# Kernel optimization log

Hardware: AMD Instinct MI355X
Metric: run time of the kernel (lower is better)

## Reference

```python
import jax, jax.numpy as jnp
import numpy as np

D_MODEL = 1024
D_KEY = 64
BATCH = 4
SEQ = 4096


def setup_inputs() -> dict:
    key = jax.random.key(0)
    kq, kk, kv, kwq, kwk, kwv = jax.random.split(key, 6)
    queries = jax.random.normal(kq, (BATCH, SEQ, D_MODEL), dtype=jnp.float32)
    keys = jax.random.normal(kk, (BATCH, SEQ, D_MODEL), dtype=jnp.float32)
    values = jax.random.normal(kv, (BATCH, SEQ, D_MODEL), dtype=jnp.float32)
    # causal mask: 1 = keep, 0 = masked out (torch masked_fill where mask==0)
    mask = jnp.tril(jnp.ones((SEQ, SEQ), dtype=jnp.int32))
    s = 1.0 / np.sqrt(D_MODEL)
    Wq = jax.random.normal(kwq, (D_MODEL, D_KEY), dtype=jnp.float32) * s
    Wk = jax.random.normal(kwk, (D_MODEL, D_KEY), dtype=jnp.float32) * s
    Wv = jax.random.normal(kwv, (D_MODEL, D_KEY), dtype=jnp.float32) * s
    return {"queries": queries, "keys": keys, "values": values,
            "mask": mask, "Wq": Wq, "Wk": Wk, "Wv": Wv}


def reference(queries, keys, values, mask, Wq, Wk, Wv):
    q = jnp.einsum('bsd,dk->bsk', queries, Wq)   # [B,S,dk]
    k = jnp.einsum('bsd,dk->bsk', keys, Wk)
    v = jnp.einsum('bsd,dk->bsk', values, Wv)
    scale = 1.0 / np.sqrt(D_KEY).astype(np.float32)
    attn = jnp.einsum('bqk,bsk->bqs', q, k) * scale  # [B,Sq,Sk]
    attn = jnp.where(mask == 0, -jnp.inf, attn)
    attn = jax.nn.softmax(attn, axis=-1)
    return jnp.einsum('bqs,bsk->bqk', attn, v)      # [B,S,dk]
```

## Files before the change

### kernel.cpp

```cpp
#include <hip/hip_runtime.h>
#include <hip/hip_bf16.h>

#define B      4
#define SEQ    4096
#define DM     1024
#define DK     64
#define NSPLIT 8

typedef __bf16 bf16x8 __attribute__((ext_vector_type(8)));
typedef __bf16 bf16x4 __attribute__((ext_vector_type(4)));
typedef float  f32x4  __attribute__((ext_vector_type(4)));

#define KSTR 72

#define QSCALE 0.1803368801111204f
#define M2BIAS 12.0f

__device__ __forceinline__ void gl_lds16(const void* g, void* l)
{
    __builtin_amdgcn_global_load_lds(
        (const __attribute__((address_space(1))) void*)g,
        (__attribute__((address_space(3))) void*)l, 16, 0, 0);
}

__global__ __launch_bounds__(256) void wt_kernel(
    const float* __restrict__ Wq, const float* __restrict__ Wk,
    const float* __restrict__ Wv, __bf16* __restrict__ Wt)
{
    const int mat = blockIdx.y;
    const float* W = (mat == 0) ? Wq : (mat == 1) ? Wk : Wv;
    const float scale = (mat == 0) ? QSCALE : 1.0f;
    const int k0 = blockIdx.x * 64;
    const int tid = threadIdx.x;

    __shared__ float t[64][65];

    const int r = tid >> 2;
    const int c = (tid & 3) * 16;
    {
        const float* src = W + (size_t)(k0 + r) * DK + c;
        #pragma unroll
        for (int j = 0; j < 4; ++j) {
            float4 a = *(const float4*)(src + j * 4);
            t[r][c + j * 4 + 0] = a.x; t[r][c + j * 4 + 1] = a.y;
            t[r][c + j * 4 + 2] = a.z; t[r][c + j * 4 + 3] = a.w;
        }
    }
    __syncthreads();
    const int n  = tid >> 2;
    const int kk = (tid & 3) * 16;
    bf16x8 b0, b1;
    #pragma unroll
    for (int j = 0; j < 8; ++j) b0[j] = (__bf16)(t[kk + j][n] * scale);
    #pragma unroll
    for (int j = 0; j < 8; ++j) b1[j] = (__bf16)(t[kk + 8 + j][n] * scale);
    __bf16* dst = Wt + (size_t)(mat * DK + n) * DM + k0 + kk;
    *(bf16x8*)(dst)     = b0;
    *(bf16x8*)(dst + 8) = b1;
}

__global__ __launch_bounds__(256) void proj_lds_kernel(
    const float* __restrict__ q_in, const float* __restrict__ k_in,
    const float* __restrict__ v_in, const __bf16* __restrict__ Wt,
    __bf16* __restrict__ qb, __bf16* __restrict__ kb,
    __bf16* __restrict__ vtb)
{
    const int m = blockIdx.y;
    const float* in = (m == 0) ? q_in : (m == 1) ? k_in : v_in;
    const __bf16* wt = Wt + (size_t)m * DK * DM;

    const int rowbase = blockIdx.x * 64;
    const int tid  = threadIdx.x;
    const int w    = tid >> 6;
    const int lane = tid & 63;
    const int quad = lane >> 4;
    const int l15  = lane & 15;

    __shared__ float  As[2][64 * 64];
    __shared__ __bf16 Ws[2][64 * 64];

    const float* asrc[4];
    #pragma unroll
    for (int i = 0; i < 4; ++i) {
        const int j = w * 4 + i;
        const int row_local = j * 4 + quad;
        asrc[i] = in + (size_t)(rowbase + row_local) * DM
                     + ((l15 ^ (row_local & 7)) << 2);
    }
    const __bf16* wsrc[2];
    const int l8 = lane >> 3, u7 = lane & 7;
    #pragma unroll
    for (int i = 0; i < 2; ++i) {
        const int j2 = w * 2 + i;
        const int n_local = j2 * 8 + l8;
        wsrc[i] = wt + (size_t)n_local * DM + ((u7 ^ (n_local & 7)) << 3);
    }

    auto stage = [&](int b, int c) {
        #pragma unroll
        for (int i = 0; i < 4; ++i)
            gl_lds16(asrc[i] + c * 64, &As[b][(w * 4 + i) * 256]);
        #pragma unroll
        for (int i = 0; i < 2; ++i)
            gl_lds16(wsrc[i] + c * 64, &Ws[b][(w * 2 + i) * 512]);
    };

    f32x4 acc[4];
    #pragma unroll
    for (int nf = 0; nf < 4; ++nf) acc[nf] = (f32x4){0.f, 0.f, 0.f, 0.f};

    stage(0, 0);

    const int row = w * 16 + l15;
    const int sw7 = l15 & 7;

    for (int c = 0; c < 16; ++c) {
        __syncthreads();
        if (c + 1 < 16) stage((c + 1) & 1, c + 1);
        const int b = c & 1;

        #pragma unroll
        for (int s = 0; s < 2; ++s) {
            const int q0 = s * 8 + quad * 2;
            float4 a0 = *(const float4*)&As[b][row * 64 + (( q0      ^ sw7) << 2)];
            float4 a1 = *(const float4*)&As[b][row * 64 + (((q0 + 1) ^ sw7) << 2)];
            bf16x8 af;
            af[0] = (__bf16)a0.x; af[1] = (__bf16)a0.y;
            af[2] = (__bf16)a0.z; af[3] = (__bf16)a0.w;
            af[4] = (__bf16)a1.x; af[5] = (__bf16)a1.y;
            af[6] = (__bf16)a1.z; af[7] = (__bf16)a1.w;
            #pragma unroll
            for (int nf = 0; nf < 4; ++nf) {
                const int n = nf * 16 + l15;
                bf16x8 wf = *(const bf16x8*)
                    &Ws[b][n * 64 + (((s * 4 + quad) ^ sw7) << 3)];
                acc[nf] = __builtin_amdgcn_mfma_f32_16x16x32_bf16(af, wf, acc[nf], 0, 0, 0);
            }
        }
    }

    if (m < 2) {
        __bf16* outb = (m == 0) ? qb : kb;
        #pragma unroll
        for (int nf = 0; nf < 4; ++nf)
            #pragma unroll
            for (int r = 0; r < 4; ++r)
                outb[(size_t)(rowbase + w * 16 + quad * 4 + r) * DK + nf * 16 + l15] =
                    (__bf16)acc[nf][r];
    } else {
        const int bb = rowbase >> 12;
        const int s0 = (rowbase & (SEQ - 1)) + w * 16 + quad * 4;
        #pragma unroll
        for (int nf = 0; nf < 4; ++nf) {
            bf16x4 v4;
            #pragma unroll
            for (int r = 0; r < 4; ++r) v4[r] = (__bf16)acc[nf][r];
            *(bf16x4*)&vtb[(size_t)(bb * DK + nf * 16 + l15) * SEQ + s0] = v4;
        }
    }
}

__global__ __launch_bounds__(256) void flash_kernel(
    const __bf16* __restrict__ qb, const __bf16* __restrict__ kb,
    const __bf16* __restrict__ vtb, __bf16* __restrict__ Opart,
    float* __restrict__ lpart)
{
    const int qt  = blockIdx.x;
    const int bb  = blockIdx.y;
    const int z   = blockIdx.z;
    const int tid = threadIdx.x;
    const int w    = tid >> 6;
    const int lane = tid & 63;
    const int quad = lane >> 4;
    const int l15  = lane & 15;

    __shared__ __bf16 Ks[64 * KSTR];
    __shared__ __bf16 Vs[64 * KSTR];
    __shared__ __bf16 Ps[4][2][16 * KSTR];

    const int qrow_base = qt * 128 + w * 32;
    const int niters = 2 * qt + 2;
    const int kt0 = (niters * z) / NSPLIT;
    const int kt1 = (niters * (z + 1)) / NSPLIT;

    bf16x8 qf[2][2];
    #pragma unroll
    for (int g = 0; g < 2; ++g) {
        const __bf16* qp = qb + ((size_t)(bb * SEQ + qrow_base + g * 16 + l15)) * DK + quad * 8;
        qf[g][0] = *(const bf16x8*)(qp);
        qf[g][1] = *(const bf16x8*)(qp + 32);
    }

    bf16x8 ones;
    #pragma unroll
    for (int j = 0; j < 8; ++j) ones[j] = (__bf16)1.0f;

    f32x4 of[2][4], lacc[2];
    #pragma unroll
    for (int g = 0; g < 2; ++g) {
        #pragma unroll
        for (int nf = 0; nf < 4; ++nf) of[g][nf] = (f32x4){0.f, 0.f, 0.f, 0.f};
        lacc[g] = (f32x4){0.f, 0.f, 0.f, 0.f};
    }

    const int sr = tid >> 2;
    const int sc = (tid & 3) * 16;
    bf16x8 kr0, kr1, vr0, vr1;
    const __bf16* kbase = kb  + ((size_t)(bb * SEQ + sr)) * DK + sc;
    const __bf16* vbase = vtb + ((size_t)(bb * DK  + sr)) * SEQ + sc;

    if (kt1 > kt0) {
        const __bf16* kg = kbase + (size_t)kt0 * 64 * DK;
        kr0 = *(const bf16x8*)(kg); kr1 = *(const bf16x8*)(kg + 8);
        const __bf16* vg = vbase + kt0 * 64;
        vr0 = *(const bf16x8*)(vg); vr1 = *(const bf16x8*)(vg + 8);
    }

    for (int kt = kt0; kt < kt1; ++kt) {
        __syncthreads();
        *(bf16x8*)&Ks[sr * KSTR + sc]     = kr0;
        *(bf16x8*)&Ks[sr * KSTR + sc + 8] = kr1;
        *(bf16x8*)&Vs[sr * KSTR + sc]     = vr0;
        *(bf16x8*)&Vs[sr * KSTR + sc + 8] = vr1;
        __syncthreads();
        if (kt + 1 < kt1) {
            const __bf16* kg = kbase + (size_t)(kt + 1) * 64 * DK;
            kr0 = *(const bf16x8*)(kg); kr1 = *(const bf16x8*)(kg + 8);
            const __bf16* vg = vbase + (kt + 1) * 64;
            vr0 = *(const bf16x8*)(vg); vr1 = *(const bf16x8*)(vg + 8);
        }

        f32x4 sf[2][4];
        #pragma unroll
        for (int g = 0; g < 2; ++g)
            #pragma unroll
            for (int nf = 0; nf < 4; ++nf)
                sf[g][nf] = (f32x4){-M2BIAS, -M2BIAS, -M2BIAS, -M2BIAS};
        #pragma unroll
        for (int nf = 0; nf < 4; ++nf) {
            #pragma unroll
            for (int ch = 0; ch < 2; ++ch) {
                bf16x8 kf = *(const bf16x8*)(&Ks[(nf * 16 + l15) * KSTR + ch * 32 + quad * 8]);
                sf[0][nf] = __builtin_amdgcn_mfma_f32_16x16x32_bf16(qf[0][ch], kf, sf[0][nf], 0, 0, 0);
                sf[1][nf] = __builtin_amdgcn_mfma_f32_16x16x32_bf16(qf[1][ch], kf, sf[1][nf], 0, 0, 0);
            }
        }

        const int kc0 = kt * 64;
        #pragma unroll
        for (int g = 0; g < 2; ++g) {
            const int r0 = qrow_base + g * 16;
            const bool dg = (kc0 + 63 > r0);
            #pragma unroll
            for (int nf = 0; nf < 4; ++nf) {
                #pragma unroll
                for (int r = 0; r < 4; ++r) {
                    float s = sf[g][nf][r];
                    if (dg) {
                        const int col = kc0 + nf * 16 + l15;
                        const int row = r0 + quad * 4 + r;
                        if (col > row) s = -1.0e9f;
                    }
                    const float p = __builtin_amdgcn_exp2f(s);
                    Ps[w][g][(quad * 4 + r) * KSTR + nf * 16 + l15] = (__bf16)p;
                }
            }
        }

        bf16x8 pf[2][2];
        #pragma unroll
        for (int g = 0; g < 2; ++g) {
            pf[g][0] = *(const bf16x8*)(&Ps[w][g][l15 * KSTR + quad * 8]);
            pf[g][1] = *(const bf16x8*)(&Ps[w][g][l15 * KSTR + 32 + quad * 8]);
            lacc[g] = __builtin_amdgcn_mfma_f32_16x16x32_bf16(pf[g][0], ones, lacc[g], 0, 0, 0);
            lacc[g] = __builtin_amdgcn_mfma_f32_16x16x32_bf16(pf[g][1], ones, lacc[g], 0, 0, 0);
        }

        #pragma unroll
        for (int nf = 0; nf < 4; ++nf) {
            #pragma unroll
            for (int ch = 0; ch < 2; ++ch) {
                bf16x8 vf = *(const bf16x8*)(&Vs[(nf * 16 + l15) * KSTR + ch * 32 + quad * 8]);
                of[0][nf] = __builtin_amdgcn_mfma_f32_16x16x32_bf16(pf[0][ch], vf, of[0][nf], 0, 0, 0);
                of[1][nf] = __builtin_amdgcn_mfma_f32_16x16x32_bf16(pf[1][ch], vf, of[1][nf], 0, 0, 0);
            }
        }
    }

    #pragma unroll
    for (int g = 0; g < 2; ++g) {
        __bf16* Op = Opart + ((size_t)(z * B + bb) * SEQ + qrow_base + g * 16) * DK;
        #pragma unroll
        for (int nf = 0; nf < 4; ++nf)
            #pragma unroll
            for (int r = 0; r < 4; ++r)
                Op[(size_t)(quad * 4 + r) * DK + nf * 16 + l15] = (__bf16)of[g][nf][r];
        if (l15 == 0) {
            const size_t base = (size_t)(z * B + bb) * SEQ + qrow_base + g * 16 + quad * 4;
            #pragma unroll
            for (int r = 0; r < 4; ++r)
                lpart[base + r] = lacc[g][r];
        }
    }
}

__global__ __launch_bounds__(256) void combine_kernel(
    const __bf16* __restrict__ Opart, const float* __restrict__ lpart,
    float* __restrict__ out)
{
    const int idx = blockIdx.x * 256 + threadIdx.x;
    const int row = idx >> 6;

    float L = 0.f, o = 0.f;
    #pragma unroll
    for (int z = 0; z < NSPLIT; ++z) {
        L += lpart[(size_t)z * (B * SEQ) + row];
        o += (float)Opart[(size_t)z * (B * SEQ) * DK + idx];
    }
    out[idx] = o / L;
}

extern "C" void kernel_launch(void* const* d_in, const int* in_sizes, int n_in,
                              void* d_out, int out_size, void* d_ws, size_t ws_size,
                              hipStream_t stream)
{
    const float* queries = (const float*)d_in[0];
    const float* keys    = (const float*)d_in[1];
    const float* values  = (const float*)d_in[2];
    const float* Wq = (const float*)d_in[4];
    const float* Wk = (const float*)d_in[5];
    const float* Wv = (const float*)d_in[6];
    float* out = (float*)d_out;

    char* p = (char*)d_ws;
    __bf16* qb  = (__bf16*)p;  p += (size_t)B * SEQ * DK * 2;
    __bf16* kb  = (__bf16*)p;  p += (size_t)B * SEQ * DK * 2;
    __bf16* vtb = (__bf16*)p;  p += (size_t)B * SEQ * DK * 2;
    __bf16* Wt  = (__bf16*)p;  p += (size_t)3 * DK * DM * 2;
    __bf16* Opart = (__bf16*)p; p += (size_t)NSPLIT * B * SEQ * DK * 2;
    float* lpart = (float*)p;   p += (size_t)NSPLIT * B * SEQ * 4;

    wt_kernel<<<dim3(DM / 64, 3), 256, 0, stream>>>(Wq, Wk, Wv, Wt);

    proj_lds_kernel<<<dim3((B * SEQ) / 64, 3), 256, 0, stream>>>(
        queries, keys, values, Wt, qb, kb, vtb);

    flash_kernel<<<dim3(SEQ / 128, B, NSPLIT), 256, 0, stream>>>(
        qb, kb, vtb, Opart, lpart);

    combine_kernel<<<(B * SEQ * DK) / 256, 256, 0, stream>>>(
        Opart, lpart, out);
}
```

Before: 279.3 us.

## Deepen projection prefetch pipeline to four LDS stages with explicit vmcnt waits

Reworks the projection GEMM's input staging. The K chunk shrinks from 64 to 32, the LDS buffers go from two to four, and loads are issued three chunks ahead. Each iteration now waits on a partial vmcnt with a raw s_barrier instead of a full __syncthreads, so global loads stay in flight across iterations and memory latency is better hidden. The cost is more barriers per tile with half the compute between them, plus a new swizzle pattern that must stay conflict-free and correct.

```diff
diff --git a/kernel.cpp b/kernel.cpp
--- a/kernel.cpp
+++ b/kernel.cpp
@@ -59,6 +59,8 @@
     *(bf16x8*)(dst + 8) = b1;
 }
 
+#define NC 32
+#define PF 3
 __global__ __launch_bounds__(256) void proj_lds_kernel(
     const float* __restrict__ q_in, const float* __restrict__ k_in,
     const float* __restrict__ v_in, const __bf16* __restrict__ Wt,
@@ -76,66 +78,56 @@
     const int quad = lane >> 4;
     const int l15  = lane & 15;
 
-    __shared__ float  As[2][64 * 64];
-    __shared__ __bf16 Ws[2][64 * 64];
-
-    const float* asrc[4];
-    #pragma unroll
-    for (int i = 0; i < 4; ++i) {
-        const int j = w * 4 + i;
-        const int row_local = j * 4 + quad;
-        asrc[i] = in + (size_t)(rowbase + row_local) * DM
-                     + ((l15 ^ (row_local & 7)) << 2);
-    }
-    const __bf16* wsrc[2];
-    const int l8 = lane >> 3, u7 = lane & 7;
-    #pragma unroll
-    for (int i = 0; i < 2; ++i) {
-        const int j2 = w * 2 + i;
-        const int n_local = j2 * 8 + l8;
-        wsrc[i] = wt + (size_t)n_local * DM + ((u7 ^ (n_local & 7)) << 3);
-    }
-
-    auto stage = [&](int b, int c) {
-        #pragma unroll
-        for (int i = 0; i < 4; ++i)
-            gl_lds16(asrc[i] + c * 64, &As[b][(w * 4 + i) * 256]);
-        #pragma unroll
-        for (int i = 0; i < 2; ++i)
-            gl_lds16(wsrc[i] + c * 64, &Ws[b][(w * 2 + i) * 512]);
+    __shared__ float  As[4][64 * 32];
+    __shared__ __bf16 Ws[4][64 * 32];
+
+    const int lr = lane >> 3, lu = lane & 7;
+    const float* asrc0 = in + (size_t)(rowbase + (w * 2 + 0) * 8 + lr) * DM
+                            + ((lu ^ lr) << 2);
+    const float* asrc1 = in + (size_t)(rowbase + (w * 2 + 1) * 8 + lr) * DM
+                            + ((lu ^ lr) << 2);
+    const int wn = lane >> 2, wu = lane & 3;
+    const __bf16* wsrc = wt + (size_t)(w * 16 + wn) * DM
+                            + (((wu ^ (wn & 3))) << 3);
+
+    auto stage = [&](int c) {
+        const int b = c & 3;
+        gl_lds16(asrc0 + c * 32, &As[b][(w * 2 + 0) * 256]);
+        gl_lds16(asrc1 + c * 32, &As[b][(w * 2 + 1) * 256]);
+        gl_lds16(wsrc  + c * 32, &Ws[b][w * 512]);
     };
 
     f32x4 acc[4];
     #pragma unroll
     for (int nf = 0; nf < 4; ++nf) acc[nf] = (f32x4){0.f, 0.f, 0.f, 0.f};
 
-    stage(0, 0);
-
-    const int row = w * 16 + l15;
-    const int sw7 = l15 & 7;
-
-    for (int c = 0; c < 16; ++c) {
-        __syncthreads();
-        if (c + 1 < 16) stage((c + 1) & 1, c + 1);
-        const int b = c & 1;
-
-        #pragma unroll
-        for (int s = 0; s < 2; ++s) {
-            const int q0 = s * 8 + quad * 2;
-            float4 a0 = *(const float4*)&As[b][row * 64 + (( q0      ^ sw7) << 2)];
-            float4 a1 = *(const float4*)&As[b][row * 64 + (((q0 + 1) ^ sw7) << 2)];
-            bf16x8 af;
-            af[0] = (__bf16)a0.x; af[1] = (__bf16)a0.y;
-            af[2] = (__bf16)a0.z; af[3] = (__bf16)a0.w;
-            af[4] = (__bf16)a1.x; af[5] = (__bf16)a1.y;
-            af[6] = (__bf16)a1.z; af[7] = (__bf16)a1.w;
-            #pragma unroll
-            for (int nf = 0; nf < 4; ++nf) {
-                const int n = nf * 16 + l15;
-                bf16x8 wf = *(const bf16x8*)
-                    &Ws[b][n * 64 + (((s * 4 + quad) ^ sw7) << 3)];
-                acc[nf] = __builtin_amdgcn_mfma_f32_16x16x32_bf16(af, wf, acc[nf], 0, 0, 0);
-            }
+    stage(0); stage(1); stage(2);
+
+    const int rowl = w * 16 + l15;
+    const int h7 = l15 & 7;
+    const int h3 = l15 & 3;
+
+    #pragma unroll
+    for (int c = 0; c < NC; ++c) {
+        if (c == NC - 1)          asm volatile("s_waitcnt vmcnt(0)" ::: "memory");
+        else if (c == NC - 2)     asm volatile("s_waitcnt vmcnt(3)" ::: "memory");
+        else                      asm volatile("s_waitcnt vmcnt(6)" ::: "memory");
+        __builtin_amdgcn_s_barrier();
+        __builtin_amdgcn_sched_barrier(0);
+        if (c + PF < NC) stage(c + PF);
+        const int b = c & 3;
+        float4 a0 = *(const float4*)&As[b][rowl * 32 + (((quad * 2)     ^ h7) << 2)];
+        float4 a1 = *(const float4*)&As[b][rowl * 32 + (((quad * 2 + 1) ^ h7) << 2)];
+        bf16x8 af;
+        af[0] = (__bf16)a0.x; af[1] = (__bf16)a0.y;
+        af[2] = (__bf16)a0.z; af[3] = (__bf16)a0.w;
+        af[4] = (__bf16)a1.x; af[5] = (__bf16)a1.y;
+        af[6] = (__bf16)a1.z; af[7] = (__bf16)a1.w;
+        #pragma unroll
+        for (int nf = 0; nf < 4; ++nf) {
+            const int n = nf * 16 + l15;
+            bf16x8 wf = *(const bf16x8*)&Ws[b][n * 32 + ((quad ^ h3) << 3)];
+            acc[nf] = __builtin_amdgcn_mfma_f32_16x16x32_bf16(af, wf, acc[nf], 0, 0, 0);
         }
     }
 
```

New measurement: 289.4 us. 3.6% more time.

## Keep full weight slice in LDS and stream activations through register prefetch

Applied to the files above, without the earlier changes.

The projection kernel now loads the entire 64x1024 bf16 weight slice into LDS once per block and streams each activation row directly from global memory into registers. A 12-deep software prefetch ring uses explicit vmcnt waits. This removes the per-chunk syncthreads and the LDS staging of fp32 activations, and it doubles block size to 512 threads covering 128 rows. In exchange it uses 128KB of LDS and many registers, which limits occupancy to one block per CU and relies on hand-counted waitcnt values.

```diff
diff --git a/kernel.cpp b/kernel.cpp
--- a/kernel.cpp
+++ b/kernel.cpp
@@ -59,7 +59,10 @@
     *(bf16x8*)(dst + 8) = b1;
 }
 
-__global__ __launch_bounds__(256) void proj_lds_kernel(
+#define PD 12
+#define WVM(n) asm volatile("s_waitcnt vmcnt(" #n ")" ::: "memory")
+
+__global__ __launch_bounds__(512, 1) void proj_lds_kernel(
     const float* __restrict__ q_in, const float* __restrict__ k_in,
     const float* __restrict__ v_in, const __bf16* __restrict__ Wt,
     __bf16* __restrict__ qb, __bf16* __restrict__ kb,
@@ -69,73 +72,73 @@
     const float* in = (m == 0) ? q_in : (m == 1) ? k_in : v_in;
     const __bf16* wt = Wt + (size_t)m * DK * DM;
 
-    const int rowbase = blockIdx.x * 64;
+    const int rowbase = blockIdx.x * 128;
     const int tid  = threadIdx.x;
     const int w    = tid >> 6;
     const int lane = tid & 63;
     const int quad = lane >> 4;
     const int l15  = lane & 15;
 
-    __shared__ float  As[2][64 * 64];
-    __shared__ __bf16 Ws[2][64 * 64];
-
-    const float* asrc[4];
-    #pragma unroll
-    for (int i = 0; i < 4; ++i) {
-        const int j = w * 4 + i;
-        const int row_local = j * 4 + quad;
-        asrc[i] = in + (size_t)(rowbase + row_local) * DM
-                     + ((l15 ^ (row_local & 7)) << 2);
-    }
-    const __bf16* wsrc[2];
-    const int l8 = lane >> 3, u7 = lane & 7;
-    #pragma unroll
-    for (int i = 0; i < 2; ++i) {
-        const int j2 = w * 2 + i;
-        const int n_local = j2 * 8 + l8;
-        wsrc[i] = wt + (size_t)n_local * DM + ((u7 ^ (n_local & 7)) << 3);
-    }
-
-    auto stage = [&](int b, int c) {
-        #pragma unroll
-        for (int i = 0; i < 4; ++i)
-            gl_lds16(asrc[i] + c * 64, &As[b][(w * 4 + i) * 256]);
-        #pragma unroll
-        for (int i = 0; i < 2; ++i)
-            gl_lds16(wsrc[i] + c * 64, &Ws[b][(w * 2 + i) * 512]);
-    };
+    __shared__ __bf16 Ws[DK * DM];
+
+    #pragma unroll
+    for (int i = 0; i < 16; ++i) {
+        const int j = w * 16 + i;
+        const int n = j >> 1;
+        const int u = ((j & 1) << 6) + lane;
+        const __bf16* src = wt + (size_t)n * DM + ((u ^ (n & 7)) << 3);
+        gl_lds16(src, (char*)Ws + j * 1024);
+    }
+    WVM(0);
+    __syncthreads();
+
+    const float* arow = in + (size_t)(rowbase + w * 16 + l15) * DM + quad * 8;
+    float4 Aa[PD], Ab[PD];
+    #pragma unroll
+    for (int d = 0; d < PD; ++d) {
+        Aa[d] = *(const float4*)(arow + d * 32);
+        Ab[d] = *(const float4*)(arow + d * 32 + 4);
+    }
 
     f32x4 acc[4];
     #pragma unroll
     for (int nf = 0; nf < 4; ++nf) acc[nf] = (f32x4){0.f, 0.f, 0.f, 0.f};
 
-    stage(0, 0);
-
-    const int row = w * 16 + l15;
-    const int sw7 = l15 & 7;
-
-    for (int c = 0; c < 16; ++c) {
-        __syncthreads();
-        if (c + 1 < 16) stage((c + 1) & 1, c + 1);
-        const int b = c & 1;
-
-        #pragma unroll
-        for (int s = 0; s < 2; ++s) {
-            const int q0 = s * 8 + quad * 2;
-            float4 a0 = *(const float4*)&As[b][row * 64 + (( q0      ^ sw7) << 2)];
-            float4 a1 = *(const float4*)&As[b][row * 64 + (((q0 + 1) ^ sw7) << 2)];
-            bf16x8 af;
-            af[0] = (__bf16)a0.x; af[1] = (__bf16)a0.y;
-            af[2] = (__bf16)a0.z; af[3] = (__bf16)a0.w;
-            af[4] = (__bf16)a1.x; af[5] = (__bf16)a1.y;
-            af[6] = (__bf16)a1.z; af[7] = (__bf16)a1.w;
-            #pragma unroll
-            for (int nf = 0; nf < 4; ++nf) {
-                const int n = nf * 16 + l15;
-                bf16x8 wf = *(const bf16x8*)
-                    &Ws[b][n * 64 + (((s * 4 + quad) ^ sw7) << 3)];
-                acc[nf] = __builtin_amdgcn_mfma_f32_16x16x32_bf16(af, wf, acc[nf], 0, 0, 0);
-            }
+    #pragma unroll
+    for (int c = 0; c < 32; ++c) {
+        const int rem = 31 - c;
+        if      (rem >= 11) WVM(22);
+        else if (rem == 10) WVM(20);
+        else if (rem ==  9) WVM(18);
+        else if (rem ==  8) WVM(16);
+        else if (rem ==  7) WVM(14);
+        else if (rem ==  6) WVM(12);
+        else if (rem ==  5) WVM(10);
+        else if (rem ==  4) WVM(8);
+        else if (rem ==  3) WVM(6);
+        else if (rem ==  2) WVM(4);
+        else if (rem ==  1) WVM(2);
+        else                WVM(0);
+        __builtin_amdgcn_sched_barrier(0);
+
+        const int s = c % PD;
+        bf16x8 af;
+        af[0] = (__bf16)Aa[s].x; af[1] = (__bf16)Aa[s].y;
+        af[2] = (__bf16)Aa[s].z; af[3] = (__bf16)Aa[s].w;
+        af[4] = (__bf16)Ab[s].x; af[5] = (__bf16)Ab[s].y;
+        af[6] = (__bf16)Ab[s].z; af[7] = (__bf16)Ab[s].w;
+
+        #pragma unroll
+        for (int nf = 0; nf < 4; ++nf) {
+            const int n = nf * 16 + l15;
+            bf16x8 wf = *(const bf16x8*)
+                ((const char*)Ws + n * 2048 + (((c * 4 + quad) ^ (n & 7)) << 4));
+            acc[nf] = __builtin_amdgcn_mfma_f32_16x16x32_bf16(af, wf, acc[nf], 0, 0, 0);
+        }
+
+        if (c + PD < 32) {
+            Aa[s] = *(const float4*)(arow + (c + PD) * 32);
+            Ab[s] = *(const float4*)(arow + (c + PD) * 32 + 4);
         }
     }
 
@@ -342,7 +345,7 @@
 
     wt_kernel<<<dim3(DM / 64, 3), 256, 0, stream>>>(Wq, Wk, Wv, Wt);
 
-    proj_lds_kernel<<<dim3((B * SEQ) / 64, 3), 256, 0, stream>>>(
+    proj_lds_kernel<<<dim3((B * SEQ) / 128, 3), 512, 0, stream>>>(
         queries, keys, values, Wt, qb, kb, vtb);
 
     flash_kernel<<<dim3(SEQ / 128, B, NSPLIT), 256, 0, stream>>>(
```

Measured after the change: 283.4 us. Within noise of the previous version (+1.4%).
